# Performance work log

Hardware: AMD Instinct MI355X
Metric: run time of the kernel (lower is better)

The kernel has to match this reference:

```python
import jax, jax.numpy as jnp
import numpy as np

N, E, P, D = 100000, 800000, 100000, 128

def setup_inputs() -> dict:
    key = jax.random.key(0)
    ks = jax.random.split(key, 24)
    def w(k, i, o):
        return jax.random.normal(k, (i, o), jnp.float32) * (1.0 / np.sqrt(i))
    inp = {
        'x': jax.random.normal(ks[0], (N, D), jnp.float32),
        'src': jax.random.randint(ks[1], (E,), 0, N, jnp.int32),
        'dst': jax.random.randint(ks[2], (E,), 0, N, jnp.int32),
        'pos_src': jax.random.randint(ks[3], (P,), 0, N, jnp.int32),
        'pos_dst': jax.random.randint(ks[4], (P,), 0, N, jnp.int32),
        'neg_src': jax.random.randint(ks[5], (P,), 0, N, jnp.int32),
        'neg_dst': jax.random.randint(ks[6], (P,), 0, N, jnp.int32),
        # SAGEConv params: fc_self, fc_neigh (+bias) per layer
        'Ws0': w(ks[7], D, D), 'Wn0': w(ks[8], D, D), 'b0': jnp.zeros((D,), jnp.float32),
        'Ws1': w(ks[9], D, D), 'Wn1': w(ks[10], D, D), 'b1': jnp.zeros((D,), jnp.float32),
        'Ws2': w(ks[11], D, D), 'Wn2': w(ks[12], D, D), 'b2': jnp.zeros((D,), jnp.float32),
        # predictor MLP: D->D->D->2
        'Wp0': w(ks[13], D, D), 'bp0': jnp.zeros((D,), jnp.float32),
        'Wp1': w(ks[14], D, D), 'bp1': jnp.zeros((D,), jnp.float32),
        'Wp2': w(ks[15], D, 2), 'bp2': jnp.zeros((2,), jnp.float32),
    }
    return inp

def _sage_layer(h, src, dst, n, Ws, Wn, b, act):
    # mean aggregation over in-neighbors (gather -> segment_sum -> divide)
    msum = jax.ops.segment_sum(h[src], dst, num_segments=n)      # [N, D]
    deg = jax.ops.segment_sum(jnp.ones_like(dst, jnp.float32), dst, num_segments=n)
    h_neigh = msum / jnp.maximum(deg, 1.0)[:, None]
    out = h @ Ws + h_neigh @ Wn + b
    return jax.nn.relu(out) if act else out

def _predict(hs, hd, Wp0, bp0, Wp1, bp1, Wp2, bp2):
    z = hs * hd
    z = jax.nn.relu(z @ Wp0 + bp0)
    z = jax.nn.relu(z @ Wp1 + bp1)
    return jax.nn.softmax(z @ Wp2 + bp2, axis=1)[:, 1]

def reference(x, src, dst, pos_src, pos_dst, neg_src, neg_dst,
              Ws0, Wn0, b0, Ws1, Wn1, b1, Ws2, Wn2, b2,
              Wp0, bp0, Wp1, bp1, Wp2, bp2):
    n = x.shape[0]
    h = _sage_layer(x, src, dst, n, Ws0, Wn0, b0, True)
    h = _sage_layer(h, src, dst, n, Ws1, Wn1, b1, True)
    h = _sage_layer(h, src, dst, n, Ws2, Wn2, b2, False)
    pos = _predict(h[pos_src], h[pos_dst], Wp0, bp0, Wp1, bp1, Wp2, bp2)
    neg = _predict(h[neg_src], h[neg_dst], Wp0, bp0, Wp1, bp1, Wp2, bp2)
    return (pos, neg)
```

## Files before the change

kernel.cpp:

```cpp
#include <hip/hip_runtime.h>
#include <cstdint>
#include <cstddef>
#include <cmath>

#define D 128

typedef short bf16x8 __attribute__((ext_vector_type(8)));
typedef float f32x4 __attribute__((ext_vector_type(4)));

__device__ __forceinline__ ushort f2b(float f) {
  uint x = __float_as_uint(f);
  uint r = ((x >> 16) & 1u) + 0x7fffu;
  return (ushort)((x + r) >> 16);
}
__device__ __forceinline__ float b2f(ushort u) {
  return __uint_as_float(((uint)u) << 16);
}

__global__ __launch_bounds__(256) void k_degree_p(const int* __restrict__ dst, int E,
    int* __restrict__ deg, float scale, int CE) {
  int part = blockIdx.x & 7, chunk = blockIdx.x >> 3;
  long base = (long)chunk * CE;
  for (int i = threadIdx.x; i < CE; i += 256) {
    long e = base + i;
    if (e < E) {
      int d = dst[e];
      int p = (int)((float)d * scale); if (p > 7) p = 7;
      if (p == part) atomicAdd(&deg[d], 1);
    }
  }
}

__global__ __launch_bounds__(256) void k_fill_p(const int* __restrict__ src,
    const int* __restrict__ dst, int E, int* __restrict__ cursor,
    int* __restrict__ csrc, float scale, int CE) {
  int part = blockIdx.x & 7, chunk = blockIdx.x >> 3;
  long base = (long)chunk * CE;
  for (int i = threadIdx.x; i < CE; i += 256) {
    long e = base + i;
    if (e < E) {
      int d = dst[e];
      int p = (int)((float)d * scale); if (p > 7) p = 7;
      if (p == part) {
        int s = src[e];
        int pos = atomicAdd(&cursor[d], 1);
        csrc[pos] = s;
      }
    }
  }
}

#define SCAN_T 256
#define SCAN_E 4
#define SCAN_CHUNK (SCAN_T * SCAN_E)

__global__ void k_scan_partial(const int* __restrict__ deg, int n, int* __restrict__ part) {
  __shared__ int s[SCAN_T];
  int base = blockIdx.x * SCAN_CHUNK;
  int sum = 0;
  for (int i = 0; i < SCAN_E; ++i) {
    int idx = base + (int)threadIdx.x * SCAN_E + i;
    if (idx < n) sum += deg[idx];
  }
  s[threadIdx.x] = sum; __syncthreads();
  for (int ofs = SCAN_T / 2; ofs > 0; ofs >>= 1) {
    if ((int)threadIdx.x < ofs) s[threadIdx.x] += s[threadIdx.x + ofs];
    __syncthreads();
  }
  if (threadIdx.x == 0) part[blockIdx.x] = s[0];
}

__global__ void k_scan_part_ex(int* __restrict__ part, int nb) {
  __shared__ int s[1024];
  int v = ((int)threadIdx.x < nb) ? part[threadIdx.x] : 0;
  s[threadIdx.x] = v; __syncthreads();
  for (int ofs = 1; ofs < 1024; ofs <<= 1) {
    int t = ((int)threadIdx.x >= ofs) ? s[threadIdx.x - ofs] : 0;
    __syncthreads();
    s[threadIdx.x] += t;
    __syncthreads();
  }
  if ((int)threadIdx.x < nb) part[threadIdx.x] = s[threadIdx.x] - v;
}

__global__ void k_scan_final(const int* __restrict__ deg, int n, const int* __restrict__ part,
                             int* __restrict__ rowptr, int* __restrict__ cursor, int E) {
  __shared__ int s[SCAN_T];
  int base = blockIdx.x * SCAN_CHUNK;
  int v[SCAN_E]; int local = 0;
  for (int i = 0; i < SCAN_E; ++i) {
    int idx = base + (int)threadIdx.x * SCAN_E + i;
    v[i] = (idx < n) ? deg[idx] : 0;
    local += v[i];
  }
  s[threadIdx.x] = local; __syncthreads();
  for (int ofs = 1; ofs < SCAN_T; ofs <<= 1) {
    int t = ((int)threadIdx.x >= ofs) ? s[threadIdx.x - ofs] : 0;
    __syncthreads();
    s[threadIdx.x] += t;
    __syncthreads();
  }
  int run = part[blockIdx.x] + s[threadIdx.x] - local;
  for (int i = 0; i < SCAN_E; ++i) {
    int idx = base + (int)threadIdx.x * SCAN_E + i;
    if (idx < n) { rowptr[idx] = run; cursor[idx] = run; }
    run += v[i];
  }
  if (blockIdx.x == 0 && threadIdx.x == 0) rowptr[n] = E;
}

__global__ void k_conv_pack(const float* __restrict__ in, ushort* __restrict__ out, int n8,
    int cb,
    const float* __restrict__ Ws0, const float* __restrict__ Wn0,
    const float* __restrict__ Ws1, const float* __restrict__ Wn1,
    const float* __restrict__ Ws2, const float* __restrict__ Wn2,
    const float* __restrict__ Wp0, const float* __restrict__ Wp1,
    ushort* __restrict__ BpL0, ushort* __restrict__ BpL1, ushort* __restrict__ BpL2,
    ushort* __restrict__ BpP0, ushort* __restrict__ BpP1) {
  int b = blockIdx.x;
  if (b < cb) {
    int i = b * 256 + threadIdx.x;
    if (i >= n8) return;
    float4 a = ((const float4*)in)[i * 2];
    float4 c = ((const float4*)in)[i * 2 + 1];
    ushort4 o0 = {f2b(a.x), f2b(a.y), f2b(a.z), f2b(a.w)};
    ushort4 o1 = {f2b(c.x), f2b(c.y), f2b(c.z), f2b(c.w)};
    ((ushort4*)out)[i * 2] = o0;
    ((ushort4*)out)[i * 2 + 1] = o1;
    return;
  }
  int o = (b - cb) * 256 + threadIdx.x;
  const float *W0, *W1; ushort* outp; int rel;
  if (o < 32768)       { W0 = Ws0; W1 = Wn0; outp = BpL0; rel = o; }
  else if (o < 65536)  { W0 = Ws1; W1 = Wn1; outp = BpL1; rel = o - 32768; }
  else if (o < 98304)  { W0 = Ws2; W1 = Wn2; outp = BpL2; rel = o - 65536; }
  else if (o < 114688) { W0 = Wp0; W1 = Wp0; outp = BpP0; rel = o - 98304; }
  else                 { W0 = Wp1; W1 = Wp1; outp = BpP1; rel = o - 114688; }
  int j = rel & 7, lane = (rel >> 3) & 63, t = (rel >> 9) & 7, ks = rel >> 12;
  int k = ks * 32 + ((lane >> 4) * 8) + j;
  int n = t * 16 + (lane & 15);
  const float* W = (k < 128) ? W0 : W1;
  int kk = (k < 128) ? k : k - 128;
  outp[rel] = f2b(W[(size_t)kk * D + n]);
}

#define SMS 136
__global__ __launch_bounds__(128, 4) void k_sage_fused(
    const ushort* __restrict__ A, const int* __restrict__ rowptr,
    const int* __restrict__ csrc, const ushort* __restrict__ Bp,
    const float* __restrict__ bias, ushort* __restrict__ out, int N, int do_relu) {
  __shared__ __align__(16) ushort smean[2][16][SMS];
  int tid = threadIdx.x, wave = tid >> 6, lane = tid & 63;
  int m = lane & 15, kg = lane >> 4;
  int g = kg, sub = m;
  int gb = g << 4;
  int row0 = (blockIdx.x * 2 + wave) * 16;
  uint hbo = (uint)(sub * 16);

  int node0 = row0 + g * 4;
  int rpv = 0;
  if (sub < 5) { int ix = node0 + sub; if (ix > N) ix = N; rpv = rowptr[ix]; }
  int beg[4], dgf[4], dd[4];
  #pragma unroll
  for (int j = 0; j < 4; ++j) {
    beg[j] = __shfl(rpv, gb + j);
    int endj = __shfl(rpv, gb + j + 1);
    dgf[j] = endj - beg[j];
    dd[j] = dgf[j] < 16 ? dgf[j] : 16;
  }
  int idxv[4];
  #pragma unroll
  for (int j = 0; j < 4; ++j) {
    int i = beg[j] + sub;
    idxv[j] = (sub < dgf[j]) ? csrc[i] : 0;
  }

  float f[4][8];
  #pragma unroll
  for (int j = 0; j < 4; ++j)
    #pragma unroll
    for (int q = 0; q < 8; ++q) f[j][q] = 0.f;

  int maxdd = dd[0];
  if (dd[1] > maxdd) maxdd = dd[1];
  if (dd[2] > maxdd) maxdd = dd[2];
  if (dd[3] > maxdd) maxdd = dd[3];

  uint off[4][4];
  #pragma unroll
  for (int j = 0; j < 4; ++j)
    #pragma unroll
    for (int k = 0; k < 4; ++k)
      off[j][k] = hbo + ((uint)__shfl(idxv[j], gb + k) << 8);

  #pragma unroll 1
  for (int e = 0; e < maxdd; e += 4) {
    bf16x8 r[4][4];
    #pragma unroll
    for (int j = 0; j < 4; ++j)
      #pragma unroll
      for (int k = 0; k < 4; ++k)
        r[j][k] = *(const bf16x8*)((const char*)A + off[j][k]);
    __builtin_amdgcn_sched_barrier(0);
    #pragma unroll
    for (int j = 0; j < 4; ++j)
      #pragma unroll
      for (int k = 0; k < 4; ++k) {
        int sl = e + 4 + k; sl = (sl > 15) ? 15 : sl;
        off[j][k] = hbo + ((uint)__shfl(idxv[j], gb + sl) << 8);
      }
    __builtin_amdgcn_sched_barrier(0);
    #pragma unroll
    for (int j = 0; j < 4; ++j) {
      #pragma unroll
      for (int k = 0; k < 4; ++k) {
        float w = (e + k < dd[j]) ? 1.0f : 0.0f;
        #pragma unroll
        for (int q = 0; q < 8; ++q) f[j][q] += w * b2f((ushort)r[j][k][q]);
      }
    }
  }
  #pragma unroll
  for (int j = 0; j < 4; ++j) {
    int endj = beg[j] + dgf[j];
    for (int i = beg[j] + 16; i < endj; ++i) {
      int s = csrc[i];
      bf16x8 v = *(const bf16x8*)((const char*)A + (hbo + ((uint)s << 8)));
      #pragma unroll
      for (int q = 0; q < 8; ++q) f[j][q] += b2f((ushort)v[q]);
    }
  }
  #pragma unroll
  for (int j = 0; j < 4; ++j) {
    float inv = (dgf[j] > 0) ? (1.0f / (float)dgf[j]) : 0.0f;
    bf16x8 o;
    #pragma unroll
    for (int q = 0; q < 8; ++q) o[q] = (short)f2b(f[j][q] * inv);
    *(bf16x8*)&smean[wave][g * 4 + j][sub * 8] = o;
  }
  asm volatile("s_waitcnt lgkmcnt(0)" ::: "memory");
  __builtin_amdgcn_sched_barrier(0);

  int ar = row0 + m; if (ar >= N) ar = N - 1;
  const ushort* a_self = A + (size_t)ar * D + kg * 8;
  f32x4 acc[8];
  #pragma unroll
  for (int t = 0; t < 8; ++t) acc[t] = f32x4{0.f, 0.f, 0.f, 0.f};
  #pragma unroll
  for (int ks = 0; ks < 8; ++ks) {
    bf16x8 af = (ks < 4) ? *(const bf16x8*)(a_self + ks * 32)
                         : *(const bf16x8*)&smean[wave][m][(ks - 4) * 32 + kg * 8];
    const ushort* bb = Bp + (size_t)ks * 4096 + lane * 8;
    #pragma unroll
    for (int t = 0; t < 8; ++t)
      acc[t] = __builtin_amdgcn_mfma_f32_16x16x32_bf16(af, *(const bf16x8*)(bb + t * 512), acc[t], 0, 0, 0);
  }
  #pragma unroll
  for (int t = 0; t < 8; ++t) {
    int c = t * 16 + m;
    float bv = bias[c];
    #pragma unroll
    for (int i = 0; i < 4; ++i) {
      int r = row0 + kg * 4 + i;
      float v = acc[t][i] + bv;
      if (do_relu) v = fmaxf(v, 0.f);
      if (r < N) out[(size_t)r * D + c] = f2b(v);
    }
  }
}

__global__ __launch_bounds__(256) void k_predict_mfma(
    const ushort* __restrict__ h,
    const int* __restrict__ ps, const int* __restrict__ pd,
    const int* __restrict__ ns, const int* __restrict__ nd,
    const ushort* __restrict__ Bp0, const float* __restrict__ bp0,
    const ushort* __restrict__ Bp1, const float* __restrict__ bp1,
    const float* __restrict__ Wp2, const float* __restrict__ bp2,
    float* __restrict__ outp, int P, int pb) {
  __shared__ __align__(16) ushort z1p[4][2048];
  int bi = blockIdx.x;
  const int* sidx; const int* didx; float* op;
  if (bi >= pb) { sidx = ns; didx = nd; op = outp + P; bi -= pb; }
  else          { sidx = ps; didx = pd; op = outp; }
  int tid = threadIdx.x;
  int wave = tid >> 6, lane = tid & 63;
  int m = lane & 15, kg = lane >> 4;
  int pair0 = bi * 64 + wave * 16;
  int prow = pair0 + m; int pr = (prow < P) ? prow : P - 1;
  int si = sidx[pr], di = didx[pr];
  const ushort* hs = h + (size_t)si * D + kg * 8;
  const ushort* hd = h + (size_t)di * D + kg * 8;
  f32x4 acc[8];
  #pragma unroll
  for (int t = 0; t < 8; ++t) acc[t] = f32x4{0.f, 0.f, 0.f, 0.f};
  #pragma unroll
  for (int ks = 0; ks < 4; ++ks) {
    bf16x8 as8 = *(const bf16x8*)(hs + ks * 32);
    bf16x8 ad8 = *(const bf16x8*)(hd + ks * 32);
    bf16x8 af;
    #pragma unroll
    for (int j = 0; j < 8; ++j) {
      float p = b2f((ushort)as8[j]) * b2f((ushort)ad8[j]);
      af[j] = (short)f2b(p);
    }
    const ushort* bb = Bp0 + (size_t)ks * 4096 + lane * 8;
    #pragma unroll
    for (int t = 0; t < 8; ++t)
      acc[t] = __builtin_amdgcn_mfma_f32_16x16x32_bf16(af, *(const bf16x8*)(bb + t * 512), acc[t], 0, 0, 0);
  }
  ushort* zp = &z1p[wave][0];
  #pragma unroll
  for (int t = 0; t < 8; ++t) {
    int c = t * 16 + m;
    float bv = bp0[c];
    int ks2 = c >> 5, kg2 = (c >> 3) & 3, j2 = c & 7;
    #pragma unroll
    for (int i = 0; i < 4; ++i) {
      float v = fmaxf(acc[t][i] + bv, 0.f);
      int l2 = kg2 * 16 + kg * 4 + i;
      zp[(ks2 * 64 + l2) * 8 + j2] = f2b(v);
    }
  }
  asm volatile("s_waitcnt lgkmcnt(0)" ::: "memory");
  __builtin_amdgcn_sched_barrier(0);
  #pragma unroll
  for (int t = 0; t < 8; ++t) acc[t] = f32x4{0.f, 0.f, 0.f, 0.f};
  #pragma unroll
  for (int ks = 0; ks < 4; ++ks) {
    bf16x8 af = *(const bf16x8*)(zp + (ks * 64 + lane) * 8);
    const ushort* bb = Bp1 + (size_t)ks * 4096 + lane * 8;
    #pragma unroll
    for (int t = 0; t < 8; ++t)
      acc[t] = __builtin_amdgcn_mfma_f32_16x16x32_bf16(af, *(const bf16x8*)(bb + t * 512), acc[t], 0, 0, 0);
  }
  float p0[4] = {0.f, 0.f, 0.f, 0.f}, p1[4] = {0.f, 0.f, 0.f, 0.f};
  #pragma unroll
  for (int t = 0; t < 8; ++t) {
    int c = t * 16 + m;
    float bv = bp1[c];
    float wa = Wp2[(size_t)c * 2], wb = Wp2[(size_t)c * 2 + 1];
    #pragma unroll
    for (int i = 0; i < 4; ++i) {
      float z = fmaxf(acc[t][i] + bv, 0.f);
      p0[i] += z * wa;
      p1[i] += z * wb;
    }
  }
  #pragma unroll
  for (int msk = 1; msk <= 8; msk <<= 1) {
    #pragma unroll
    for (int i = 0; i < 4; ++i) {
      p0[i] += __shfl_xor(p0[i], msk);
      p1[i] += __shfl_xor(p1[i], msk);
    }
  }
  if (m == 0) {
    float c0 = bp2[0], c1 = bp2[1];
    #pragma unroll
    for (int i = 0; i < 4; ++i) {
      int r = pair0 + kg * 4 + i;
      if (r < P) {
        float l0 = p0[i] + c0, l1 = p1[i] + c1;
        op[r] = 1.0f / (1.0f + expf(l0 - l1));
      }
    }
  }
}

extern "C" void kernel_launch(void* const* d_in, const int* in_sizes, int n_in,
                              void* d_out, int out_size, void* d_ws, size_t ws_size,
                              hipStream_t stream) {
  const float* x       = (const float*)d_in[0];
  const int*   src     = (const int*)d_in[1];
  const int*   dst     = (const int*)d_in[2];
  const int*   pos_src = (const int*)d_in[3];
  const int*   pos_dst = (const int*)d_in[4];
  const int*   neg_src = (const int*)d_in[5];
  const int*   neg_dst = (const int*)d_in[6];
  const float* Ws0 = (const float*)d_in[7],  *Wn0 = (const float*)d_in[8],  *b0 = (const float*)d_in[9];
  const float* Ws1 = (const float*)d_in[10], *Wn1 = (const float*)d_in[11], *b1 = (const float*)d_in[12];
  const float* Ws2 = (const float*)d_in[13], *Wn2 = (const float*)d_in[14], *b2 = (const float*)d_in[15];
  const float* Wp0 = (const float*)d_in[16], *bp0 = (const float*)d_in[17];
  const float* Wp1 = (const float*)d_in[18], *bp1 = (const float*)d_in[19];
  const float* Wp2 = (const float*)d_in[20], *bp2 = (const float*)d_in[21];
  const int N = in_sizes[0] / D;
  const int E = in_sizes[1];
  const int P = in_sizes[3];
  float* outp = (float*)d_out;

  char* ws = (char*)d_ws;
  size_t off = 0;
  auto alloc = [&](size_t bytes) -> void* {
    void* p = ws + off;
    off += (bytes + 255) & ~(size_t)255;
    return p;
  };
  ushort* xb    = (ushort*)alloc((size_t)N * D * 2);
  ushort* h1    = (ushort*)alloc((size_t)N * D * 2);
  ushort* h2    = (ushort*)alloc((size_t)N * D * 2);
  ushort* BpL0  = (ushort*)alloc(256 * D * 2);
  ushort* BpL1  = (ushort*)alloc(256 * D * 2);
  ushort* BpL2  = (ushort*)alloc(256 * D * 2);
  ushort* BpP0  = (ushort*)alloc(128 * D * 2);
  ushort* BpP1  = (ushort*)alloc(128 * D * 2);
  int*    deg    = (int*)alloc((size_t)N * 4);
  int*    rowptr = (int*)alloc((size_t)(N + 1) * 4);
  int*    cursor = (int*)alloc((size_t)N * 4);
  int*    part   = (int*)alloc(4096);
  int*    csrc   = (int*)alloc((size_t)E * 4);
  (void)ws_size; (void)n_in; (void)out_size;

  const float pscale = 8.0f / (float)N;
  const int CB = 96;
  const int CE = (E + CB - 1) / CB;

  hipMemsetAsync(deg, 0, (size_t)N * 4, stream);
  k_degree_p<<<8 * CB, 256, 0, stream>>>(dst, E, deg, pscale, CE);
  int nb = (N + SCAN_CHUNK - 1) / SCAN_CHUNK;
  k_scan_partial<<<nb, SCAN_T, 0, stream>>>(deg, N, part);
  k_scan_part_ex<<<1, 1024, 0, stream>>>(part, nb);
  k_scan_final<<<nb, SCAN_T, 0, stream>>>(deg, N, part, rowptr, cursor, E);
  k_fill_p<<<8 * CB, 256, 0, stream>>>(src, dst, E, cursor, csrc, pscale, CE);

  int n8 = N * D / 8;
  int cb = (n8 + 255) / 256;
  k_conv_pack<<<cb + 512, 256, 0, stream>>>(x, xb, n8, cb,
                                            Ws0, Wn0, Ws1, Wn1, Ws2, Wn2, Wp0, Wp1,
                                            BpL0, BpL1, BpL2, BpP0, BpP1);

  int gemb = (N + 31) / 32;
  k_sage_fused<<<gemb, 128, 0, stream>>>(xb, rowptr, csrc, BpL0, b0, h1, N, 1);
  k_sage_fused<<<gemb, 128, 0, stream>>>(h1, rowptr, csrc, BpL1, b1, h2, N, 1);
  k_sage_fused<<<gemb, 128, 0, stream>>>(h2, rowptr, csrc, BpL2, b2, xb, N, 0);

  int pb = (P + 63) / 64;
  k_predict_mfma<<<2 * pb, 256, 0, stream>>>(xb, pos_src, pos_dst, neg_src, neg_dst,
                                             BpP0, bp0, BpP1, bp1, Wp2, bp2, outp, P, pb);
}
```

Measured before the change: 441.6 us.

## Merge degree count with conversion kernel, fold scan pass, stage predictor gathers via LDS

```diff
diff --git a/kernel.cpp b/kernel.cpp
--- a/kernel.cpp
+++ b/kernel.cpp
@@ -17,18 +17,60 @@
   return __uint_as_float(((uint)u) << 16);
 }
 
-__global__ __launch_bounds__(256) void k_degree_p(const int* __restrict__ dst, int E,
-    int* __restrict__ deg, float scale, int CE) {
-  int part = blockIdx.x & 7, chunk = blockIdx.x >> 3;
-  long base = (long)chunk * CE;
-  for (int i = threadIdx.x; i < CE; i += 256) {
-    long e = base + i;
-    if (e < E) {
-      int d = dst[e];
-      int p = (int)((float)d * scale); if (p > 7) p = 7;
-      if (p == part) atomicAdd(&deg[d], 1);
-    }
-  }
+__device__ __forceinline__ void gl2lds16(const void* g, void* l) {
+  __builtin_amdgcn_global_load_lds(
+      (__attribute__((address_space(1))) void*)const_cast<void*>(g),
+      (__attribute__((address_space(3))) void*)l, 16, 0, 0);
+}
+
+__global__ __launch_bounds__(256) void k_degree_conv(
+    const int* __restrict__ dst, int E, int* __restrict__ deg, float scale, int CE,
+    const float* __restrict__ in, ushort* __restrict__ outx, int n8, int cb,
+    const float* __restrict__ Ws0, const float* __restrict__ Wn0,
+    const float* __restrict__ Ws1, const float* __restrict__ Wn1,
+    const float* __restrict__ Ws2, const float* __restrict__ Wn2,
+    const float* __restrict__ Wp0, const float* __restrict__ Wp1,
+    ushort* __restrict__ BpL0, ushort* __restrict__ BpL1, ushort* __restrict__ BpL2,
+    ushort* __restrict__ BpP0, ushort* __restrict__ BpP1) {
+  int b = blockIdx.x;
+  if (b < 768) {
+    int part = b & 7, chunk = b >> 3;
+    long base = (long)chunk * CE;
+    for (int i = threadIdx.x; i < CE; i += 256) {
+      long e = base + i;
+      if (e < E) {
+        int d = dst[e];
+        int p = (int)((float)d * scale); if (p > 7) p = 7;
+        if (p == part) atomicAdd(&deg[d], 1);
+      }
+    }
+    return;
+  }
+  int b2 = b - 768;
+  if (b2 < cb) {
+    int i = b2 * 256 + threadIdx.x;
+    if (i >= n8) return;
+    float4 a = ((const float4*)in)[i * 2];
+    float4 c = ((const float4*)in)[i * 2 + 1];
+    ushort4 o0 = {f2b(a.x), f2b(a.y), f2b(a.z), f2b(a.w)};
+    ushort4 o1 = {f2b(c.x), f2b(c.y), f2b(c.z), f2b(c.w)};
+    ((ushort4*)outx)[i * 2] = o0;
+    ((ushort4*)outx)[i * 2 + 1] = o1;
+    return;
+  }
+  int o = (b2 - cb) * 256 + threadIdx.x;
+  const float *W0, *W1; ushort* outp; int rel;
+  if (o < 32768)       { W0 = Ws0; W1 = Wn0; outp = BpL0; rel = o; }
+  else if (o < 65536)  { W0 = Ws1; W1 = Wn1; outp = BpL1; rel = o - 32768; }
+  else if (o < 98304)  { W0 = Ws2; W1 = Wn2; outp = BpL2; rel = o - 65536; }
+  else if (o < 114688) { W0 = Wp0; W1 = Wp0; outp = BpP0; rel = o - 98304; }
+  else                 { W0 = Wp1; W1 = Wp1; outp = BpP1; rel = o - 114688; }
+  int j = rel & 7, lane = (rel >> 3) & 63, t = (rel >> 9) & 7, ks = rel >> 12;
+  int k = ks * 32 + ((lane >> 4) * 8) + j;
+  int n = t * 16 + (lane & 15);
+  const float* W = (k < 128) ? W0 : W1;
+  int kk = (k < 128) ? k : k - 128;
+  outp[rel] = f2b(W[(size_t)kk * D + n]);
 }
 
 __global__ __launch_bounds__(256) void k_fill_p(const int* __restrict__ src,
@@ -70,22 +112,21 @@
   if (threadIdx.x == 0) part[blockIdx.x] = s[0];
 }
 
-__global__ void k_scan_part_ex(int* __restrict__ part, int nb) {
-  __shared__ int s[1024];
-  int v = ((int)threadIdx.x < nb) ? part[threadIdx.x] : 0;
-  s[threadIdx.x] = v; __syncthreads();
-  for (int ofs = 1; ofs < 1024; ofs <<= 1) {
-    int t = ((int)threadIdx.x >= ofs) ? s[threadIdx.x - ofs] : 0;
+__global__ void k_scan_final(const int* __restrict__ deg, int n, const int* __restrict__ part,
+                             int nb, int* __restrict__ rowptr, int* __restrict__ cursor, int E) {
+  __shared__ int s[SCAN_T];
+  __shared__ int pbase;
+  {
+    int v = 0;
+    for (int t = (int)threadIdx.x; t < (int)blockIdx.x; t += SCAN_T) v += part[t];
+    s[threadIdx.x] = v; __syncthreads();
+    for (int ofs = SCAN_T / 2; ofs > 0; ofs >>= 1) {
+      if ((int)threadIdx.x < ofs) s[threadIdx.x] += s[threadIdx.x + ofs];
+      __syncthreads();
+    }
+    if (threadIdx.x == 0) pbase = s[0];
     __syncthreads();
-    s[threadIdx.x] += t;
-    __syncthreads();
-  }
-  if ((int)threadIdx.x < nb) part[threadIdx.x] = s[threadIdx.x] - v;
-}
-
-__global__ void k_scan_final(const int* __restrict__ deg, int n, const int* __restrict__ part,
-                             int* __restrict__ rowptr, int* __restrict__ cursor, int E) {
-  __shared__ int s[SCAN_T];
+  }
   int base = blockIdx.x * SCAN_CHUNK;
   int v[SCAN_E]; int local = 0;
   for (int i = 0; i < SCAN_E; ++i) {
@@ -100,48 +141,13 @@
     s[threadIdx.x] += t;
     __syncthreads();
   }
-  int run = part[blockIdx.x] + s[threadIdx.x] - local;
+  int run = pbase + s[threadIdx.x] - local;
   for (int i = 0; i < SCAN_E; ++i) {
     int idx = base + (int)threadIdx.x * SCAN_E + i;
     if (idx < n) { rowptr[idx] = run; cursor[idx] = run; }
     run += v[i];
   }
   if (blockIdx.x == 0 && threadIdx.x == 0) rowptr[n] = E;
-}
-
-__global__ void k_conv_pack(const float* __restrict__ in, ushort* __restrict__ out, int n8,
-    int cb,
-    const float* __restrict__ Ws0, const float* __restrict__ Wn0,
-    const float* __restrict__ Ws1, const float* __restrict__ Wn1,
-    const float* __restrict__ Ws2, const float* __restrict__ Wn2,
-    const float* __restrict__ Wp0, const float* __restrict__ Wp1,
-    ushort* __restrict__ BpL0, ushort* __restrict__ BpL1, ushort* __restrict__ BpL2,
-    ushort* __restrict__ BpP0, ushort* __restrict__ BpP1) {
-  int b = blockIdx.x;
-  if (b < cb) {
-    int i = b * 256 + threadIdx.x;
-    if (i >= n8) return;
-    float4 a = ((const float4*)in)[i * 2];
-    float4 c = ((const float4*)in)[i * 2 + 1];
-    ushort4 o0 = {f2b(a.x), f2b(a.y), f2b(a.z), f2b(a.w)};
-    ushort4 o1 = {f2b(c.x), f2b(c.y), f2b(c.z), f2b(c.w)};
-    ((ushort4*)out)[i * 2] = o0;
-    ((ushort4*)out)[i * 2 + 1] = o1;
-    return;
-  }
-  int o = (b - cb) * 256 + threadIdx.x;
-  const float *W0, *W1; ushort* outp; int rel;
-  if (o < 32768)       { W0 = Ws0; W1 = Wn0; outp = BpL0; rel = o; }
-  else if (o < 65536)  { W0 = Ws1; W1 = Wn1; outp = BpL1; rel = o - 32768; }
-  else if (o < 98304)  { W0 = Ws2; W1 = Wn2; outp = BpL2; rel = o - 65536; }
-  else if (o < 114688) { W0 = Wp0; W1 = Wp0; outp = BpP0; rel = o - 98304; }
-  else                 { W0 = Wp1; W1 = Wp1; outp = BpP1; rel = o - 114688; }
-  int j = rel & 7, lane = (rel >> 3) & 63, t = (rel >> 9) & 7, ks = rel >> 12;
-  int k = ks * 32 + ((lane >> 4) * 8) + j;
-  int n = t * 16 + (lane & 15);
-  const float* W = (k < 128) ? W0 : W1;
-  int kk = (k < 128) ? k : k - 128;
-  outp[rel] = f2b(W[(size_t)kk * D + n]);
 }
 
 #define SMS 136
@@ -269,7 +275,7 @@
   }
 }
 
-__global__ __launch_bounds__(256) void k_predict_mfma(
+__global__ __launch_bounds__(256, 5) void k_predict_mfma(
     const ushort* __restrict__ h,
     const int* __restrict__ ps, const int* __restrict__ pd,
     const int* __restrict__ ns, const int* __restrict__ nd,
@@ -277,7 +283,7 @@
     const ushort* __restrict__ Bp1, const float* __restrict__ bp1,
     const float* __restrict__ Wp2, const float* __restrict__ bp2,
     float* __restrict__ outp, int P, int pb) {
-  __shared__ __align__(16) ushort z1p[4][2048];
+  __shared__ __align__(1024) ushort slab[4][4096];
   int bi = blockIdx.x;
   const int* sidx; const int* didx; float* op;
   if (bi >= pb) { sidx = ns; didx = nd; op = outp + P; bi -= pb; }
@@ -288,15 +294,38 @@
   int pair0 = bi * 64 + wave * 16;
   int prow = pair0 + m; int pr = (prow < P) ? prow : P - 1;
   int si = sidx[pr], di = didx[pr];
-  const ushort* hs = h + (size_t)si * D + kg * 8;
-  const ushort* hd = h + (size_t)di * D + kg * 8;
+  char* sl = (char*)&slab[wave][0];
+
+  {
+    int rsub = lane >> 4;
+    #pragma unroll
+    for (int q = 0; q < 4; ++q) {
+      int rr = q * 4 + rsub;
+      int ir = __shfl(si, rr);
+      const char* g = (const char*)h + ((size_t)(uint)ir << 8)
+                      + (uint)((((lane & 15) ^ (rr & 7)) << 4));
+      gl2lds16(g, sl + (q << 10));
+    }
+    #pragma unroll
+    for (int q = 0; q < 4; ++q) {
+      int rr = q * 4 + rsub;
+      int ir = __shfl(di, rr);
+      const char* g = (const char*)h + ((size_t)(uint)ir << 8)
+                      + (uint)((((lane & 15) ^ (rr & 7)) << 4));
+      gl2lds16(g, sl + 4096 + (q << 10));
+    }
+  }
+  __syncthreads();
+
   f32x4 acc[8];
   #pragma unroll
   for (int t = 0; t < 8; ++t) acc[t] = f32x4{0.f, 0.f, 0.f, 0.f};
   #pragma unroll
   for (int ks = 0; ks < 4; ++ks) {
-    bf16x8 as8 = *(const bf16x8*)(hs + ks * 32);
-    bf16x8 ad8 = *(const bf16x8*)(hd + ks * 32);
+    int slot = (ks * 4 + kg) ^ (m & 7);
+    const char* rbase = sl + m * 256 + slot * 16;
+    bf16x8 as8 = *(const bf16x8*)rbase;
+    bf16x8 ad8 = *(const bf16x8*)(rbase + 4096);
     bf16x8 af;
     #pragma unroll
     for (int j = 0; j < 8; ++j) {
@@ -308,7 +337,7 @@
     for (int t = 0; t < 8; ++t)
       acc[t] = __builtin_amdgcn_mfma_f32_16x16x32_bf16(af, *(const bf16x8*)(bb + t * 512), acc[t], 0, 0, 0);
   }
-  ushort* zp = &z1p[wave][0];
+  ushort* zp = (ushort*)sl;
   #pragma unroll
   for (int t = 0; t < 8; ++t) {
     int c = t * 16 + m;
@@ -415,18 +444,18 @@
   const int CE = (E + CB - 1) / CB;
 
   hipMemsetAsync(deg, 0, (size_t)N * 4, stream);
-  k_degree_p<<<8 * CB, 256, 0, stream>>>(dst, E, deg, pscale, CE);
+  int n8 = N * D / 8;
+  int cb = (n8 + 255) / 256;
+  k_degree_conv<<<8 * CB + cb + 512, 256, 0, stream>>>(
+      dst, E, deg, pscale, CE,
+      x, xb, n8, cb,
+      Ws0, Wn0, Ws1, Wn1, Ws2, Wn2, Wp0, Wp1,
+      BpL0, BpL1, BpL2, BpP0, BpP1);
+
   int nb = (N + SCAN_CHUNK - 1) / SCAN_CHUNK;
   k_scan_partial<<<nb, SCAN_T, 0, stream>>>(deg, N, part);
-  k_scan_part_ex<<<1, 1024, 0, stream>>>(part, nb);
-  k_scan_final<<<nb, SCAN_T, 0, stream>>>(deg, N, part, rowptr, cursor, E);
+  k_scan_final<<<nb, SCAN_T, 0, stream>>>(deg, N, part, nb, rowptr, cursor, E);
   k_fill_p<<<8 * CB, 256, 0, stream>>>(src, dst, E, cursor, csrc, pscale, CE);
-
-  int n8 = N * D / 8;
-  int cb = (n8 + 255) / 256;
-  k_conv_pack<<<cb + 512, 256, 0, stream>>>(x, xb, n8, cb,
-                                            Ws0, Wn0, Ws1, Wn1, Ws2, Wn2, Wp0, Wp1,
-                                            BpL0, BpL1, BpL2, BpP0, BpP1);
 
   int gemb = (N + 31) / 32;
   k_sage_fused<<<gemb, 128, 0, stream>>>(xb, rowptr, csrc, BpL0, b0, h1, N, 1);
```

Result: no change. 435.4 us, median of 2 (-1.4%).
